# Kernel tuning notes

Measured on AMD Instinct MI355X. Metric: run time of the kernel, lower is better.

## Reference

```python
import jax, jax.numpy as jnp
import numpy as np

B, T, D, W = 8, 2048, 512, 5  # batch, time, hidden_dim, window_size


def setup_inputs() -> dict:
    key = jax.random.key(0)
    k1, k2, k3, k4, k5 = jax.random.split(key, 5)
    outputs = jax.random.normal(k1, (B, T, D), dtype=jnp.float32)
    # torch.nn.Linear default init: U(-1/sqrt(fan_in), 1/sqrt(fan_in))
    s1 = 1.0 / np.sqrt(W * D)
    s2 = 1.0 / np.sqrt((W + 1) * D)
    W_mlp = jax.random.uniform(k2, (D, W * D), jnp.float32, -s1, s1)
    b_mlp = jax.random.uniform(k3, (D,), jnp.float32, -s1, s1)
    W_gate = jax.random.uniform(k4, (D, (W + 1) * D), jnp.float32, -s2, s2)
    b_gate = jax.random.uniform(k5, (D,), jnp.float32, -s2, s2)
    return {"outputs": outputs, "W_mlp": W_mlp, "b_mlp": b_mlp,
            "W_gate": W_gate, "b_gate": b_gate}


def _window_gather(outputs, win):
    """Replicates get_subseq_idx_list + zero padding appended at the end.
    Valid indices are the sorted in-range members of [t-h, t+h]; because
    invalid indices only occur contiguously at the left (t near 0) or right
    (t near T-1) edge, padding-at-end == shift valid entries to the front.
    Returns [B, T, W, D] with zeros in padded slots."""
    Bv, Tv, Dv = outputs.shape
    h = win // 2
    t = jnp.arange(Tv)[:, None]            # [T,1]
    j = jnp.arange(win)[None, :]           # [1,W]
    shift = jnp.maximum(0, h - t)          # left-edge shift
    idx = t - h + j + shift                # [T,W]
    nvalid = jnp.minimum(t + h, Tv - 1) - jnp.maximum(t - h, 0) + 1
    mask = (j < nvalid)                    # [T,W]
    idx = jnp.where(mask, idx, 0)
    winf = outputs[:, idx, :]              # [B,T,W,D]
    return winf * mask[None, :, :, None].astype(outputs.dtype)


def reference(outputs, W_mlp, b_mlp, W_gate, b_gate):
    Bv, Tv, Dv = outputs.shape
    win = W_mlp.shape[1] // Dv             # window size
    scale = 1.0 / jnp.sqrt(jnp.asarray(Dv, outputs.dtype))
    winf = _window_gather(outputs, win)            # [B,T,W,D]
    winf_t = jnp.transpose(winf, (1, 0, 2, 3))     # [T,B,W,D] for scan

    def step(state, w):                            # state: [B,D], w: [B,W,D]
        scores = jnp.einsum('bd,bwd->bw', state, w) * scale
        prob = jax.nn.softmax(scores, axis=-1)     # zeros included, as in torch
        attn = jnp.einsum('bw,bwd->bd', prob, w)   # new prev_state
        flat = w.reshape(Bv, win * Dv)
        mlp = flat @ W_mlp.T + b_mlp
        gate = jax.nn.sigmoid(jnp.concatenate([flat, attn], axis=-1) @ W_gate.T + b_gate)
        out = mlp + attn * gate
        return out, out

    state0 = jnp.zeros((Bv, Dv), dtype=outputs.dtype)
    _, ys = jax.lax.scan(step, state0, winf_t)     # ys: [T,B,D]
    return jnp.transpose(ys, (1, 0, 2))            # [B,T,D]
```

## Files before the change

### kernel.cpp

```cpp
#include <hip/hip_runtime.h>

#define Bq 8
#define Tq 2048
#define Dq 512

typedef __attribute__((ext_vector_type(8))) _Float16 f16x8;
typedef __attribute__((ext_vector_type(8))) short u16x8;
typedef __attribute__((ext_vector_type(4))) float f32x4;

__global__ __launch_bounds__(256) void cvt_f16split(
    const float* __restrict__ s, ushort* __restrict__ hi,
    ushort* __restrict__ lo, int n8) {
  int i = blockIdx.x * 256 + threadIdx.x;
  if (i >= n8) return;
  const float4* sp = reinterpret_cast<const float4*>(s) + i * 2;
  float4 a = sp[0], b = sp[1];
  float x[8] = {a.x, a.y, a.z, a.w, b.x, b.y, b.z, b.w};
  ushort h[8], l[8];
#pragma unroll
  for (int e = 0; e < 8; e++) {
    float xs = x[e] * 256.0f;
    _Float16 hh = (_Float16)xs;
    _Float16 ll = (_Float16)(xs - (float)hh);
    h[e] = *(ushort*)&hh;
    l[e] = *(ushort*)&ll;
  }
  *reinterpret_cast<u16x8*>(hi + (size_t)i * 8) = *reinterpret_cast<u16x8*>(h);
  *reinterpret_cast<u16x8*>(lo + (size_t)i * 8) = *reinterpret_cast<u16x8*>(l);
}

template <int CTRL>
__device__ __forceinline__ float dppadd(float v) {
  int r = __builtin_amdgcn_update_dpp(0, __float_as_int(v), CTRL, 0xF, 0xF, true);
  return v + __int_as_float(r);
}
__device__ __forceinline__ float wave_sum_bcast(float v) {
  v = dppadd<0x111>(v);
  v = dppadd<0x112>(v);
  v = dppadd<0x114>(v);
  v = dppadd<0x118>(v);
  v = dppadd<0x142>(v);
  v = dppadd<0x143>(v);
  return __int_as_float(__builtin_amdgcn_readlane(__float_as_int(v), 63));
}

__device__ __forceinline__ void load_row(const float* __restrict__ base, int r,
                                         int lane, float4& a, float4& b) {
  const float* p = base + (size_t)r * Dq + lane * 4;
  a = *reinterpret_cast<const float4*>(p);
  b = *reinterpret_cast<const float4*>(p + 256);
}

__device__ __forceinline__ float dot8(const float4& xa, const float4& xb,
                                      const float4& ya, const float4& yb) {
  float s = xa.x * ya.x;
  s = fmaf(xa.y, ya.y, s); s = fmaf(xa.z, ya.z, s); s = fmaf(xa.w, ya.w, s);
  s = fmaf(xb.x, yb.x, s); s = fmaf(xb.y, yb.y, s);
  s = fmaf(xb.z, yb.z, s); s = fmaf(xb.w, yb.w, s);
  return s;
}

__device__ __forceinline__ float4 gate_out(const float4& pm, const float4& pg,
                                           const float4& at, const float4& gs) {
  float4 o;
  o.x = fmaf(at.x, __fdividef(1.f, 1.f + __expf(-(pg.x + gs.x))), pm.x);
  o.y = fmaf(at.y, __fdividef(1.f, 1.f + __expf(-(pg.y + gs.y))), pm.y);
  o.z = fmaf(at.z, __fdividef(1.f, 1.f + __expf(-(pg.z + gs.z))), pm.z);
  o.w = fmaf(at.w, __fdividef(1.f, 1.f + __expf(-(pg.w + gs.w))), pm.w);
  return o;
}

#define WSUM4(dst, arr)                                                        \
  dst.x = q0 * arr[S0].x + q1 * arr[S1].x + q2 * arr[S2].x + q3 * arr[S3].x +  \
          q4 * arr[S4].x;                                                      \
  dst.y = q0 * arr[S0].y + q1 * arr[S1].y + q2 * arr[S2].y + q3 * arr[S3].y +  \
          q4 * arr[S4].y;                                                      \
  dst.z = q0 * arr[S0].z + q1 * arr[S1].z + q2 * arr[S2].z + q3 * arr[S3].z +  \
          q4 * arr[S4].z;                                                      \
  dst.w = q0 * arr[S0].w + q1 * arr[S1].w + q2 * arr[S2].w + q3 * arr[S3].w +  \
          q4 * arr[S4].w;

__device__ __forceinline__ void wait_band(int* done, int idx, int target) {
  int it = 0;
  while (__hip_atomic_load(&done[idx], __ATOMIC_ACQUIRE,
                           __HIP_MEMORY_SCOPE_AGENT) < target) {
    __builtin_amdgcn_s_sleep(8);
    if (++it > (1 << 22)) break;
  }
}

template <int S0, int S1, int S2, int S3, int S4, int SLOT, int SLW, bool FLUSH>
__device__ __forceinline__ void scan_step(
    int t, float m3, float m4,
    const float* __restrict__ ob, const float* __restrict__ Gb,
    const float* __restrict__ Pgb, const float* __restrict__ pmb,
    float* __restrict__ po,
    float4 (&owA)[8], float4 (&owB)[8], float4 (&gwA)[8], float4 (&gwB)[8],
    float4 (&pmA)[8], float4 (&pmB)[8], float4 (&pgA)[8], float4 (&pgB)[8],
    float4& stA, float4& stB, int lane, float (*outl)[Dq],
    int* done, int bb, int& bandReady) {
  int rw = t + 5; if (rw > Tq - 1) rw = Tq - 1;
  int band = rw >> 7;
  if (band > bandReady) {
    wait_band(done, bb + band, 12);
    bandReady = band;
  }
  __builtin_amdgcn_sched_barrier(0);
  load_row(ob,  rw, lane, owA[SLW], owB[SLW]);
  load_row(Gb,  rw, lane, gwA[SLW], gwB[SLW]);
  load_row(pmb, rw, lane, pmA[SLW], pmB[SLW]);
  load_row(Pgb, rw, lane, pgA[SLW], pgB[SLW]);
  __builtin_amdgcn_sched_barrier(0);

  float s0 = dot8(stA, stB, owA[S0], owB[S0]);
  float s1 = dot8(stA, stB, owA[S1], owB[S1]);
  float s2 = dot8(stA, stB, owA[S2], owB[S2]);
  float s3 = dot8(stA, stB, owA[S3], owB[S3]);
  float s4 = dot8(stA, stB, owA[S4], owB[S4]);
  const float scale = 0.04419417382415922f;
  s0 = wave_sum_bcast(s0) * scale;
  s1 = wave_sum_bcast(s1) * scale;
  s2 = wave_sum_bcast(s2) * scale;
  s3 = wave_sum_bcast(s3) * (scale * m3);
  s4 = wave_sum_bcast(s4) * (scale * m4);

  float mx = fmaxf(fmaxf(fmaxf(s0, s1), fmaxf(s2, s3)), s4);
  float e0 = __expf(s0 - mx), e1 = __expf(s1 - mx), e2 = __expf(s2 - mx);
  float e3 = __expf(s3 - mx), e4 = __expf(s4 - mx);
  float inv = __fdividef(1.0f, e0 + e1 + e2 + e3 + e4);
  float q0 = e0 * inv, q1 = e1 * inv, q2 = e2 * inv;
  float q3 = e3 * inv * m3, q4 = e4 * inv * m4;

  float4 atA, atB, gsA, gsB;
  WSUM4(atA, owA); WSUM4(atB, owB);
  WSUM4(gsA, gwA); WSUM4(gsB, gwB);

  stA = gate_out(pmA[SLOT], pgA[SLOT], atA, gsA);
  stB = gate_out(pmB[SLOT], pgB[SLOT], atB, gsB);

  reinterpret_cast<float4*>(&outl[SLOT][0])[lane] = stA;
  reinterpret_cast<float4*>(&outl[SLOT][256])[lane] = stB;

  if (FLUSH) {
#pragma unroll
    for (int s = 0; s < 8; s++) {
      float4 va = reinterpret_cast<float4*>(&outl[s][0])[lane];
      float4 vb = reinterpret_cast<float4*>(&outl[s][256])[lane];
      float* dst = po + (size_t)(t - 7 + s) * Dq + lane * 4;
      *reinterpret_cast<float4*>(dst) = va;
      *reinterpret_cast<float4*>(dst + 256) = vb;
    }
  }
}

__global__ __launch_bounds__(256, 1) void fused_kernel(
    const float* __restrict__ O,
    const ushort* __restrict__ Ohi, const ushort* __restrict__ Olo,
    const ushort* __restrict__ Wmh, const ushort* __restrict__ Wml,
    const ushort* __restrict__ Wgh, const ushort* __restrict__ Wgl,
    const float* __restrict__ bm, const float* __restrict__ bg,
    float* __restrict__ Pg, float* __restrict__ Gm,
    float* __restrict__ out, int* __restrict__ done) {
  __shared__ float outl[8][Dq];

  if (blockIdx.x < 8) {
    if (threadIdx.x >= 64) return;
    int b = blockIdx.x;
    int lane = threadIdx.x;
    int bb = b * 16;
    const float* ob  = O   + (size_t)b * Tq * Dq;
    const float* Gb  = Gm  + (size_t)b * Tq * Dq;
    const float* Pgb = Pg  + (size_t)b * Tq * Dq;
    const float* pmb = out + (size_t)b * Tq * Dq;
    float* po = out + (size_t)b * Tq * Dq;

    int bandReady = -1;
    wait_band(done, bb + 0, 12);
    bandReady = 0;
    __builtin_amdgcn_sched_barrier(0);

    float4 owA[8], owB[8], gwA[8], gwB[8], pmA[8], pmB[8], pgA[8], pgB[8];
    float4 stA = make_float4(0.f, 0.f, 0.f, 0.f);
    float4 stB = make_float4(0.f, 0.f, 0.f, 0.f);
#pragma unroll
    for (int r = 0; r < 5; r++) {
      load_row(ob,  r, lane, owA[r], owB[r]);
      load_row(Gb,  r, lane, gwA[r], gwB[r]);
      load_row(pmb, r, lane, pmA[r], pmB[r]);
      load_row(Pgb, r, lane, pgA[r], pgB[r]);
    }

    scan_step<0,1,2,3,4, 0, 5, false>(0, 0.f, 0.f, ob, Gb, Pgb, pmb, po,
        owA,owB,gwA,gwB,pmA,pmB,pgA,pgB, stA,stB, lane, outl, done, bb, bandReady);
    scan_step<0,1,2,3,4, 1, 6, false>(1, 1.f, 0.f, ob, Gb, Pgb, pmb, po,
        owA,owB,gwA,gwB,pmA,pmB,pgA,pgB, stA,stB, lane, outl, done, bb, bandReady);
    for (int tb = 2; tb <= 2034; tb += 8) {
      scan_step<0,1,2,3,4, 2, 7, false>(tb+0, 1.f, 1.f, ob, Gb, Pgb, pmb, po,
          owA,owB,gwA,gwB,pmA,pmB,pgA,pgB, stA,stB, lane, outl, done, bb, bandReady);
      scan_step<1,2,3,4,5, 3, 0, false>(tb+1, 1.f, 1.f, ob, Gb, Pgb, pmb, po,
          owA,owB,gwA,gwB,pmA,pmB,pgA,pgB, stA,stB, lane, outl, done, bb, bandReady);
      scan_step<2,3,4,5,6, 4, 1, false>(tb+2, 1.f, 1.f, ob, Gb, Pgb, pmb, po,
          owA,owB,gwA,gwB,pmA,pmB,pgA,pgB, stA,stB, lane, outl, done, bb, bandReady);
      scan_step<3,4,5,6,7, 5, 2, false>(tb+3, 1.f, 1.f, ob, Gb, Pgb, pmb, po,
          owA,owB,gwA,gwB,pmA,pmB,pgA,pgB, stA,stB, lane, outl, done, bb, bandReady);
      scan_step<4,5,6,7,0, 6, 3, false>(tb+4, 1.f, 1.f, ob, Gb, Pgb, pmb, po,
          owA,owB,gwA,gwB,pmA,pmB,pgA,pgB, stA,stB, lane, outl, done, bb, bandReady);
      scan_step<5,6,7,0,1, 7, 4, true >(tb+5, 1.f, 1.f, ob, Gb, Pgb, pmb, po,
          owA,owB,gwA,gwB,pmA,pmB,pgA,pgB, stA,stB, lane, outl, done, bb, bandReady);
      scan_step<6,7,0,1,2, 0, 5, false>(tb+6, 1.f, 1.f, ob, Gb, Pgb, pmb, po,
          owA,owB,gwA,gwB,pmA,pmB,pgA,pgB, stA,stB, lane, outl, done, bb, bandReady);
      scan_step<7,0,1,2,3, 1, 6, false>(tb+7, 1.f, 1.f, ob, Gb, Pgb, pmb, po,
          owA,owB,gwA,gwB,pmA,pmB,pgA,pgB, stA,stB, lane, outl, done, bb, bandReady);
    }
    scan_step<0,1,2,3,4, 2, 7, false>(2042, 1.f, 1.f, ob, Gb, Pgb, pmb, po,
        owA,owB,gwA,gwB,pmA,pmB,pgA,pgB, stA,stB, lane, outl, done, bb, bandReady);
    scan_step<1,2,3,4,5, 3, 0, false>(2043, 1.f, 1.f, ob, Gb, Pgb, pmb, po,
        owA,owB,gwA,gwB,pmA,pmB,pgA,pgB, stA,stB, lane, outl, done, bb, bandReady);
    scan_step<2,3,4,5,6, 4, 1, false>(2044, 1.f, 1.f, ob, Gb, Pgb, pmb, po,
        owA,owB,gwA,gwB,pmA,pmB,pgA,pgB, stA,stB, lane, outl, done, bb, bandReady);
    scan_step<3,4,5,6,7, 5, 2, false>(2045, 1.f, 1.f, ob, Gb, Pgb, pmb, po,
        owA,owB,gwA,gwB,pmA,pmB,pgA,pgB, stA,stB, lane, outl, done, bb, bandReady);
    scan_step<4,5,6,7,0, 6, 3, false>(2046, 1.f, 0.f, ob, Gb, Pgb, pmb, po,
        owA,owB,gwA,gwB,pmA,pmB,pgA,pgB, stA,stB, lane, outl, done, bb, bandReady);
    scan_step<5,6,7,0,1, 7, 4, true >(2047, 0.f, 0.f, ob, Gb, Pgb, pmb, po,
        owA,owB,gwA,gwB,pmA,pmB,pgA,pgB, stA,stB, lane, outl, done, bb, bandReady);
    return;
  }

  int g = blockIdx.x - 8;
  int band = g / 96;
  int rem = g % 96;
  int bat = rem / 12;
  int role = rem % 12;
  int bt0 = (bat * 16 + band) * 128;
  int gb = bat * Tq;
  int t0 = bt0 % Tq;

  int tid = threadIdx.x;
  int l = tid & 63, w = tid >> 6;
  int wm = w >> 1, wn = w & 1;
  int r16 = l & 15, kg = l >> 4;

  f32x4 acc[4][4] = {};
  const f16x8 zz = {0, 0, 0, 0, 0, 0, 0, 0};

  if (role >= 8) {
    int by = role - 8;
    const ushort *bph[4], *bpl[4];
    int ncol[4];
#pragma unroll
    for (int ni = 0; ni < 4; ni++) {
      int n_g = by * 128 + wn * 64 + ni * 16 + r16;
      ncol[ni] = n_g;
      size_t off = (size_t)n_g * 3072 + 2560 + kg * 8;
      bph[ni] = Wgh + off; bpl[ni] = Wgl + off;
    }
    const ushort *aph[4], *apl[4];
#pragma unroll
    for (int mi = 0; mi < 4; mi++) {
      size_t off = (size_t)(bt0 + wm * 64 + mi * 16 + r16) * Dq + kg * 8;
      aph[mi] = Ohi + off; apl[mi] = Olo + off;
    }
#pragma unroll 4
    for (int ks = 0; ks < 16; ks++) {
      f16x8 Ah[4], Al[4], Bh[4], Bl[4];
#pragma unroll
      for (int mi = 0; mi < 4; mi++) {
        Ah[mi] = *(const f16x8*)aph[mi]; aph[mi] += 32;
        Al[mi] = *(const f16x8*)apl[mi]; apl[mi] += 32;
      }
#pragma unroll
      for (int ni = 0; ni < 4; ni++) {
        Bh[ni] = *(const f16x8*)bph[ni]; bph[ni] += 32;
        Bl[ni] = *(const f16x8*)bpl[ni]; bpl[ni] += 32;
      }
#pragma unroll
      for (int mi = 0; mi < 4; mi++)
#pragma unroll
        for (int ni = 0; ni < 4; ni++) {
          acc[mi][ni] = __builtin_amdgcn_mfma_f32_16x16x32_f16(Ah[mi], Bh[ni], acc[mi][ni], 0, 0, 0);
          acc[mi][ni] = __builtin_amdgcn_mfma_f32_16x16x32_f16(Al[mi], Bh[ni], acc[mi][ni], 0, 0, 0);
          acc[mi][ni] = __builtin_amdgcn_mfma_f32_16x16x32_f16(Ah[mi], Bl[ni], acc[mi][ni], 0, 0, 0);
        }
    }
    const float SC = 1.0f / 65536.0f;
#pragma unroll
    for (int ni = 0; ni < 4; ni++) {
#pragma unroll
      for (int mi = 0; mi < 4; mi++) {
        int rowb = bt0 + wm * 64 + mi * 16 + kg * 4;
#pragma unroll
        for (int rr = 0; rr < 4; rr++)
          Gm[(size_t)(rowb + rr) * Dq + ncol[ni]] = acc[mi][ni][rr] * SC;
      }
    }
  } else {
    int by = role;
    const ushort *bph[4], *bpl[4];
    int ncol[4];
#pragma unroll
    for (int ni = 0; ni < 4; ni++) {
      int n_g = by * 128 + wn * 64 + ni * 16 + r16;
      ncol[ni] = n_g;
      size_t off;
      if (by < 4) { off = (size_t)n_g * 2560 + kg * 8; bph[ni] = Wmh + off; bpl[ni] = Wml + off; }
      else { off = (size_t)(n_g - 512) * 3072 + kg * 8; bph[ni] = Wgh + off; bpl[ni] = Wgl + off; }
    }
    int arow[4][5];
    uint vmask[4];
#pragma unroll
    for (int mi = 0; mi < 4; mi++) {
      int t = t0 + wm * 64 + mi * 16 + r16;
      int sh = 2 - t; if (sh < 0) sh = 0;
      int hi2 = t + 2; if (hi2 > Tq - 1) hi2 = Tq - 1;
      int lo2 = t - 2; if (lo2 < 0) lo2 = 0;
      int nv = hi2 - lo2 + 1;
      uint vm = 0;
#pragma unroll
      for (int j = 0; j < 5; j++) {
        int r = t - 2 + j + sh;
        if (r > Tq - 1) r = Tq - 1;
        arow[mi][j] = gb + r;
        if (j < nv) vm |= (1u << j);
      }
      vmask[mi] = vm;
    }
#pragma unroll
    for (int j = 0; j < 5; j++) {
      const ushort *aph[4], *apl[4];
      bool v[4];
#pragma unroll
      for (int mi = 0; mi < 4; mi++) {
        size_t off = (size_t)arow[mi][j] * Dq + kg * 8;
        aph[mi] = Ohi + off; apl[mi] = Olo + off;
        v[mi] = (vmask[mi] >> j) & 1u;
      }
#pragma unroll 4
      for (int ks = 0; ks < 16; ks++) {
        f16x8 Ah[4], Al[4], Bh[4], Bl[4];
#pragma unroll
        for (int mi = 0; mi < 4; mi++) {
          f16x8 th = *(const f16x8*)aph[mi]; aph[mi] += 32;
          f16x8 tl = *(const f16x8*)apl[mi]; apl[mi] += 32;
          Ah[mi] = v[mi] ? th : zz;
          Al[mi] = v[mi] ? tl : zz;
        }
#pragma unroll
        for (int ni = 0; ni < 4; ni++) {
          Bh[ni] = *(const f16x8*)bph[ni]; bph[ni] += 32;
          Bl[ni] = *(const f16x8*)bpl[ni]; bpl[ni] += 32;
        }
#pragma unroll
        for (int mi = 0; mi < 4; mi++)
#pragma unroll
          for (int ni = 0; ni < 4; ni++) {
            acc[mi][ni] = __builtin_amdgcn_mfma_f32_16x16x32_f16(Ah[mi], Bh[ni], acc[mi][ni], 0, 0, 0);
            acc[mi][ni] = __builtin_amdgcn_mfma_f32_16x16x32_f16(Al[mi], Bh[ni], acc[mi][ni], 0, 0, 0);
            acc[mi][ni] = __builtin_amdgcn_mfma_f32_16x16x32_f16(Ah[mi], Bl[ni], acc[mi][ni], 0, 0, 0);
          }
      }
    }
    const float SC = 1.0f / 65536.0f;
    float* dst = (by < 4) ? out : Pg;
    const float* bias = (by < 4) ? bm : bg;
#pragma unroll
    for (int ni = 0; ni < 4; ni++) {
      int oc = (by < 4) ? ncol[ni] : ncol[ni] - 512;
      float bi = bias[oc];
#pragma unroll
      for (int mi = 0; mi < 4; mi++) {
        int rowb = bt0 + wm * 64 + mi * 16 + kg * 4;
#pragma unroll
        for (int rr = 0; rr < 4; rr++)
          dst[(size_t)(rowb + rr) * Dq + oc] = fmaf(acc[mi][ni][rr], SC, bi);
      }
    }
  }

  __threadfence();
  __syncthreads();
  if (tid == 0) {
    __hip_atomic_fetch_add(&done[bat * 16 + band], 1, __ATOMIC_RELEASE,
                           __HIP_MEMORY_SCOPE_AGENT);
  }
}

__global__ __launch_bounds__(256) void gemm_pre(
    const float* __restrict__ O, const float* __restrict__ Wm,
    const float* __restrict__ Wg, const float* __restrict__ bm,
    const float* __restrict__ bg, float* __restrict__ Pm,
    float* __restrict__ Pg, float* __restrict__ Gm, int mode) {
  const int BM = 128, BN = 128, BK = 16;
  __shared__ float As[BK][132];
  __shared__ float Bs[BK][132];
  int tidx = threadIdx.x;
  int bt0 = blockIdx.x * BM;
  int b = bt0 / Tq;
  int t0 = bt0 % Tq;
  int n0 = blockIdx.y * BN;
  int K = mode ? Dq : 5 * Dq;
  int tx = tidx % 16, ty = tidx / 16, lr = tidx >> 2, lc = (tidx & 3) * 4;
  float acc[8][8];
#pragma unroll
  for (int i = 0; i < 8; i++)
#pragma unroll
    for (int j = 0; j < 8; j++) acc[i][j] = 0.f;
  for (int kb = 0; kb < K; kb += BK) {
#pragma unroll
    for (int h = 0; h < 2; h++) {
      int m = lr + h * 64;
      int t = t0 + m;
      float4 av;
      if (mode == 0) {
        int j = kb >> 9;
        int kcol = (kb & 511) + lc;
        int sh = 2 - t; if (sh < 0) sh = 0;
        int r = t - 2 + j + sh;
        int hi = t + 2; if (hi > Tq - 1) hi = Tq - 1;
        int lo2 = t - 2; if (lo2 < 0) lo2 = 0;
        int nv = hi - lo2 + 1;
        if (j < nv) av = *reinterpret_cast<const float4*>(O + ((size_t)b * Tq + r) * Dq + kcol);
        else av = make_float4(0.f, 0.f, 0.f, 0.f);
      } else {
        av = *reinterpret_cast<const float4*>(O + ((size_t)b * Tq + t) * Dq + kb + lc);
      }
      As[lc + 0][m] = av.x; As[lc + 1][m] = av.y;
      As[lc + 2][m] = av.z; As[lc + 3][m] = av.w;
    }
#pragma unroll
    for (int h = 0; h < 2; h++) {
      int n = lr + h * 64;
      int gn = n0 + n;
      const float* wrow;
      int col;
      if (mode == 0) {
        if (gn < 512) { wrow = Wm + (size_t)gn * 2560; col = kb + lc; }
        else          { wrow = Wg + (size_t)(gn - 512) * 3072; col = kb + lc; }
      } else {
        wrow = Wg + (size_t)gn * 3072; col = 2560 + kb + lc;
      }
      float4 bv = *reinterpret_cast<const float4*>(wrow + col);
      Bs[lc + 0][n] = bv.x; Bs[lc + 1][n] = bv.y;
      Bs[lc + 2][n] = bv.z; Bs[lc + 3][n] = bv.w;
    }
    __syncthreads();
#pragma unroll
    for (int kk = 0; kk < BK; kk++) {
      float a[8], bb[8];
      float4 a0 = *reinterpret_cast<float4*>(&As[kk][ty * 8]);
      float4 a1 = *reinterpret_cast<float4*>(&As[kk][ty * 8 + 4]);
      float4 b0 = *reinterpret_cast<float4*>(&Bs[kk][tx * 8]);
      float4 b1 = *reinterpret_cast<float4*>(&Bs[kk][tx * 8 + 4]);
      a[0]=a0.x; a[1]=a0.y; a[2]=a0.z; a[3]=a0.w; a[4]=a1.x; a[5]=a1.y; a[6]=a1.z; a[7]=a1.w;
      bb[0]=b0.x; bb[1]=b0.y; bb[2]=b0.z; bb[3]=b0.w; bb[4]=b1.x; bb[5]=b1.y; bb[6]=b1.z; bb[7]=b1.w;
#pragma unroll
      for (int i = 0; i < 8; i++)
#pragma unroll
        for (int j = 0; j < 8; j++) acc[i][j] = fmaf(a[i], bb[j], acc[i][j]);
    }
    __syncthreads();
  }
  int gn = n0 + tx * 8;
  float bias[8];
  float* dstbase;
  int coloff;
  if (mode == 0) {
    if (gn < 512) {
#pragma unroll
      for (int j = 0; j < 8; j++) bias[j] = bm[gn + j];
      dstbase = Pm; coloff = gn;
    } else {
#pragma unroll
      for (int j = 0; j < 8; j++) bias[j] = bg[gn - 512 + j];
      dstbase = Pg; coloff = gn - 512;
    }
  } else {
#pragma unroll
    for (int j = 0; j < 8; j++) bias[j] = 0.f;
    dstbase = Gm; coloff = gn;
  }
#pragma unroll
  for (int i = 0; i < 8; i++) {
    int bt = bt0 + ty * 8 + i;
    float4 v0 = make_float4(acc[i][0] + bias[0], acc[i][1] + bias[1],
                            acc[i][2] + bias[2], acc[i][3] + bias[3]);
    float4 v1 = make_float4(acc[i][4] + bias[4], acc[i][5] + bias[5],
                            acc[i][6] + bias[6], acc[i][7] + bias[7]);
    float4* d = reinterpret_cast<float4*>(dstbase + (size_t)bt * Dq + coloff);
    d[0] = v0;
    d[1] = v1;
  }
}

__global__ __launch_bounds__(64, 1) void scan_only(
    const float* __restrict__ O, const float* __restrict__ Gm,
    const float* __restrict__ Pg, const float* __restrict__ Pm,
    float* __restrict__ out, int* __restrict__ done) {
  __shared__ float outl[8][Dq];
  int b = blockIdx.x;
  int lane = threadIdx.x;
  int bb = b * 16;
  const float* ob  = O  + (size_t)b * Tq * Dq;
  const float* Gb  = Gm + (size_t)b * Tq * Dq;
  const float* Pgb = Pg + (size_t)b * Tq * Dq;
  const float* pmb = Pm + (size_t)b * Tq * Dq;
  float* po = out + (size_t)b * Tq * Dq;
  int bandReady = 15;

  float4 owA[8], owB[8], gwA[8], gwB[8], pmA[8], pmB[8], pgA[8], pgB[8];
  float4 stA = make_float4(0.f, 0.f, 0.f, 0.f);
  float4 stB = make_float4(0.f, 0.f, 0.f, 0.f);
#pragma unroll
  for (int r = 0; r < 5; r++) {
    load_row(ob,  r, lane, owA[r], owB[r]);
    load_row(Gb,  r, lane, gwA[r], gwB[r]);
    load_row(pmb, r, lane, pmA[r], pmB[r]);
    load_row(Pgb, r, lane, pgA[r], pgB[r]);
  }
  scan_step<0,1,2,3,4, 0, 5, false>(0, 0.f, 0.f, ob, Gb, Pgb, pmb, po,
      owA,owB,gwA,gwB,pmA,pmB,pgA,pgB, stA,stB, lane, outl, done, bb, bandReady);
  scan_step<0,1,2,3,4, 1, 6, false>(1, 1.f, 0.f, ob, Gb, Pgb, pmb, po,
      owA,owB,gwA,gwB,pmA,pmB,pgA,pgB, stA,stB, lane, outl, done, bb, bandReady);
  for (int tb = 2; tb <= 2034; tb += 8) {
    scan_step<0,1,2,3,4, 2, 7, false>(tb+0, 1.f, 1.f, ob, Gb, Pgb, pmb, po,
        owA,owB,gwA,gwB,pmA,pmB,pgA,pgB, stA,stB, lane, outl, done, bb, bandReady);
    scan_step<1,2,3,4,5, 3, 0, false>(tb+1, 1.f, 1.f, ob, Gb, Pgb, pmb, po,
        owA,owB,gwA,gwB,pmA,pmB,pgA,pgB, stA,stB, lane, outl, done, bb, bandReady);
    scan_step<2,3,4,5,6, 4, 1, false>(tb+2, 1.f, 1.f, ob, Gb, Pgb, pmb, po,
        owA,owB,gwA,gwB,pmA,pmB,pgA,pgB, stA,stB, lane, outl, done, bb, bandReady);
    scan_step<3,4,5,6,7, 5, 2, false>(tb+3, 1.f, 1.f, ob, Gb, Pgb, pmb, po,
        owA,owB,gwA,gwB,pmA,pmB,pgA,pgB, stA,stB, lane, outl, done, bb, bandReady);
    scan_step<4,5,6,7,0, 6, 3, false>(tb+4, 1.f, 1.f, ob, Gb, Pgb, pmb, po,
        owA,owB,gwA,gwB,pmA,pmB,pgA,pgB, stA,stB, lane, outl, done, bb, bandReady);
    scan_step<5,6,7,0,1, 7, 4, true >(tb+5, 1.f, 1.f, ob, Gb, Pgb, pmb, po,
        owA,owB,gwA,gwB,pmA,pmB,pgA,pgB, stA,stB, lane, outl, done, bb, bandReady);
    scan_step<6,7,0,1,2, 0, 5, false>(tb+6, 1.f, 1.f, ob, Gb, Pgb, pmb, po,
        owA,owB,gwA,gwB,pmA,pmB,pgA,pgB, stA,stB, lane, outl, done, bb, bandReady);
    scan_step<7,0,1,2,3, 1, 6, false>(tb+7, 1.f, 1.f, ob, Gb, Pgb, pmb, po,
        owA,owB,gwA,gwB,pmA,pmB,pgA,pgB, stA,stB, lane, outl, done, bb, bandReady);
  }
  scan_step<0,1,2,3,4, 2, 7, false>(2042, 1.f, 1.f, ob, Gb, Pgb, pmb, po,
      owA,owB,gwA,gwB,pmA,pmB,pgA,pgB, stA,stB, lane, outl, done, bb, bandReady);
  scan_step<1,2,3,4,5, 3, 0, false>(2043, 1.f, 1.f, ob, Gb, Pgb, pmb, po,
      owA,owB,gwA,gwB,pmA,pmB,pgA,pgB, stA,stB, lane, outl, done, bb, bandReady);
  scan_step<2,3,4,5,6, 4, 1, false>(2044, 1.f, 1.f, ob, Gb, Pgb, pmb, po,
      owA,owB,gwA,gwB,pmA,pmB,pgA,pgB, stA,stB, lane, outl, done, bb, bandReady);
  scan_step<3,4,5,6,7, 5, 2, false>(2045, 1.f, 1.f, ob, Gb, Pgb, pmb, po,
      owA,owB,gwA,gwB,pmA,pmB,pgA,pgB, stA,stB, lane, outl, done, bb, bandReady);
  scan_step<4,5,6,7,0, 6, 3, false>(2046, 1.f, 0.f, ob, Gb, Pgb, pmb, po,
      owA,owB,gwA,gwB,pmA,pmB,pgA,pgB, stA,stB, lane, outl, done, bb, bandReady);
  scan_step<5,6,7,0,1, 7, 4, true >(2047, 0.f, 0.f, ob, Gb, Pgb, pmb, po,
      owA,owB,gwA,gwB,pmA,pmB,pgA,pgB, stA,stB, lane, outl, done, bb, bandReady);
}

extern "C" void kernel_launch(void* const* d_in, const int* in_sizes, int n_in,
                              void* d_out, int out_size, void* d_ws, size_t ws_size,
                              hipStream_t stream) {
  const float* O  = (const float*)d_in[0];
  const float* Wm = (const float*)d_in[1];
  const float* bm = (const float*)d_in[2];
  const float* Wg = (const float*)d_in[3];
  const float* bg = (const float*)d_in[4];
  float* out = (float*)d_out;

  const size_t NTOT = (size_t)Bq * Tq * Dq;
  const size_t NWM = 512 * 2560, NWG = 512 * 3072;
  float* Pg = (float*)d_ws;
  float* Gm = Pg + NTOT;
  ushort* OHI = (ushort*)(Gm + NTOT);
  ushort* OLO = OHI + NTOT;
  ushort* WMH = OLO + NTOT;
  ushort* WML = WMH + NWM;
  ushort* WGH = WML + NWM;
  ushort* WGL = WGH + NWG;
  int* done = (int*)(WGL + NWG);

  size_t need = 2 * NTOT * 4 + 2 * (NTOT + NWM + NWG) * 2 + 128 * 4;
  if (ws_size >= need) {
    hipMemsetAsync(done, 0, 128 * 4, stream);
    cvt_f16split<<<dim3((NTOT / 8 + 255) / 256), dim3(256), 0, stream>>>(O, OHI, OLO, NTOT / 8);
    cvt_f16split<<<dim3((NWM / 8 + 255) / 256), dim3(256), 0, stream>>>(Wm, WMH, WML, NWM / 8);
    cvt_f16split<<<dim3((NWG / 8 + 255) / 256), dim3(256), 0, stream>>>(Wg, WGH, WGL, NWG / 8);
    fused_kernel<<<dim3(8 + 16 * 96), dim3(256), 0, stream>>>(
        O, OHI, OLO, WMH, WML, WGH, WGL, bm, bg, Pg, Gm, out, done);
  } else {
    bool sep = ws_size >= (size_t)(3 * NTOT * 4 + 128 * 4);
    float* Pm = sep ? (Gm + NTOT) : out;
    int* done2 = sep ? (int*)(Pm + NTOT) : (int*)(Gm + NTOT);
    hipMemsetAsync(done2, 12, 128 * 4, stream);
    gemm_pre<<<dim3(128, 8), dim3(256), 0, stream>>>(O, Wm, Wg, bm, bg, Pm, Pg, Gm, 0);
    gemm_pre<<<dim3(128, 4), dim3(256), 0, stream>>>(O, Wm, Wg, bm, bg, Pm, Pg, Gm, 1);
    scan_only<<<dim3(Bq), dim3(64), 0, stream>>>(O, Gm, Pg, Pm, out, done2);
  }
}
```

Baseline: 1.779 ms.

## Split recurrent scan across four waves with LDS cross-wave score reduction

The sequential scan per batch now uses all four waves of the block instead of one. Each wave handles 128 of the 512 hidden dims and each thread holds two elements rather than eight. The five attention scores are reduced within each wave, exchanged through a small double-buffered shared array, and combined after a block barrier on every timestep. The LDS output staging and periodic flush are dropped in favour of a direct float2 store per step. This cuts per-thread work and register pressure on the latency-bound recurrence, at the cost of a block-wide barrier and an LDS round trip on every step.

```diff
diff --git a/kernel.cpp b/kernel.cpp
--- a/kernel.cpp
+++ b/kernel.cpp
@@ -44,42 +44,6 @@
   return __int_as_float(__builtin_amdgcn_readlane(__float_as_int(v), 63));
 }
 
-__device__ __forceinline__ void load_row(const float* __restrict__ base, int r,
-                                         int lane, float4& a, float4& b) {
-  const float* p = base + (size_t)r * Dq + lane * 4;
-  a = *reinterpret_cast<const float4*>(p);
-  b = *reinterpret_cast<const float4*>(p + 256);
-}
-
-__device__ __forceinline__ float dot8(const float4& xa, const float4& xb,
-                                      const float4& ya, const float4& yb) {
-  float s = xa.x * ya.x;
-  s = fmaf(xa.y, ya.y, s); s = fmaf(xa.z, ya.z, s); s = fmaf(xa.w, ya.w, s);
-  s = fmaf(xb.x, yb.x, s); s = fmaf(xb.y, yb.y, s);
-  s = fmaf(xb.z, yb.z, s); s = fmaf(xb.w, yb.w, s);
-  return s;
-}
-
-__device__ __forceinline__ float4 gate_out(const float4& pm, const float4& pg,
-                                           const float4& at, const float4& gs) {
-  float4 o;
-  o.x = fmaf(at.x, __fdividef(1.f, 1.f + __expf(-(pg.x + gs.x))), pm.x);
-  o.y = fmaf(at.y, __fdividef(1.f, 1.f + __expf(-(pg.y + gs.y))), pm.y);
-  o.z = fmaf(at.z, __fdividef(1.f, 1.f + __expf(-(pg.z + gs.z))), pm.z);
-  o.w = fmaf(at.w, __fdividef(1.f, 1.f + __expf(-(pg.w + gs.w))), pm.w);
-  return o;
-}
-
-#define WSUM4(dst, arr)                                                        \
-  dst.x = q0 * arr[S0].x + q1 * arr[S1].x + q2 * arr[S2].x + q3 * arr[S3].x +  \
-          q4 * arr[S4].x;                                                      \
-  dst.y = q0 * arr[S0].y + q1 * arr[S1].y + q2 * arr[S2].y + q3 * arr[S3].y +  \
-          q4 * arr[S4].y;                                                      \
-  dst.z = q0 * arr[S0].z + q1 * arr[S1].z + q2 * arr[S2].z + q3 * arr[S3].z +  \
-          q4 * arr[S4].z;                                                      \
-  dst.w = q0 * arr[S0].w + q1 * arr[S1].w + q2 * arr[S2].w + q3 * arr[S3].w +  \
-          q4 * arr[S4].w;
-
 __device__ __forceinline__ void wait_band(int* done, int idx, int target) {
   int it = 0;
   while (__hip_atomic_load(&done[idx], __ATOMIC_ACQUIRE,
@@ -89,16 +53,15 @@
   }
 }
 
-template <int S0, int S1, int S2, int S3, int S4, int SLOT, int SLW, bool FLUSH>
-__device__ __forceinline__ void scan_step(
-    int t, float m3, float m4,
+template <int S0, int S1, int S2, int S3, int S4, int SLOT, int SLW>
+__device__ __forceinline__ void scan_step4(
+    int t, float m3, float m4, int lane, int w, int dbase,
     const float* __restrict__ ob, const float* __restrict__ Gb,
     const float* __restrict__ Pgb, const float* __restrict__ pmb,
-    float* __restrict__ po,
-    float4 (&owA)[8], float4 (&owB)[8], float4 (&gwA)[8], float4 (&gwB)[8],
-    float4 (&pmA)[8], float4 (&pmB)[8], float4 (&pgA)[8], float4 (&pgB)[8],
-    float4& stA, float4& stB, int lane, float (*outl)[Dq],
-    int* done, int bb, int& bandReady) {
+    float* __restrict__ po, float (*red)[5][4],
+    int* done, int bb, int& bandReady,
+    float2 (&ow)[8], float2 (&gw)[8], float2 (&pm)[8], float2 (&pg)[8],
+    float2& st) {
   int rw = t + 5; if (rw > Tq - 1) rw = Tq - 1;
   int band = rw >> 7;
   if (band > bandReady) {
@@ -106,51 +69,66 @@
     bandReady = band;
   }
   __builtin_amdgcn_sched_barrier(0);
-  load_row(ob,  rw, lane, owA[SLW], owB[SLW]);
-  load_row(Gb,  rw, lane, gwA[SLW], gwB[SLW]);
-  load_row(pmb, rw, lane, pmA[SLW], pmB[SLW]);
-  load_row(Pgb, rw, lane, pgA[SLW], pgB[SLW]);
+  ow[SLW] = *(const float2*)(ob  + (size_t)rw * Dq + dbase);
+  gw[SLW] = *(const float2*)(Gb  + (size_t)rw * Dq + dbase);
+  pm[SLW] = *(const float2*)(pmb + (size_t)rw * Dq + dbase);
+  pg[SLW] = *(const float2*)(Pgb + (size_t)rw * Dq + dbase);
   __builtin_amdgcn_sched_barrier(0);
 
-  float s0 = dot8(stA, stB, owA[S0], owB[S0]);
-  float s1 = dot8(stA, stB, owA[S1], owB[S1]);
-  float s2 = dot8(stA, stB, owA[S2], owB[S2]);
-  float s3 = dot8(stA, stB, owA[S3], owB[S3]);
-  float s4 = dot8(stA, stB, owA[S4], owB[S4]);
   const float scale = 0.04419417382415922f;
-  s0 = wave_sum_bcast(s0) * scale;
-  s1 = wave_sum_bcast(s1) * scale;
-  s2 = wave_sum_bcast(s2) * scale;
-  s3 = wave_sum_bcast(s3) * (scale * m3);
-  s4 = wave_sum_bcast(s4) * (scale * m4);
-
-  float mx = fmaxf(fmaxf(fmaxf(s0, s1), fmaxf(s2, s3)), s4);
-  float e0 = __expf(s0 - mx), e1 = __expf(s1 - mx), e2 = __expf(s2 - mx);
-  float e3 = __expf(s3 - mx), e4 = __expf(s4 - mx);
+  float s0 = st.x * ow[S0].x; s0 = fmaf(st.y, ow[S0].y, s0);
+  float s1 = st.x * ow[S1].x; s1 = fmaf(st.y, ow[S1].y, s1);
+  float s2 = st.x * ow[S2].x; s2 = fmaf(st.y, ow[S2].y, s2);
+  float s3 = st.x * ow[S3].x; s3 = fmaf(st.y, ow[S3].y, s3);
+  float s4 = st.x * ow[S4].x; s4 = fmaf(st.y, ow[S4].y, s4);
+  s0 = wave_sum_bcast(s0);
+  s1 = wave_sum_bcast(s1);
+  s2 = wave_sum_bcast(s2);
+  s3 = wave_sum_bcast(s3);
+  s4 = wave_sum_bcast(s4);
+  s0 *= scale; s1 *= scale; s2 *= scale;
+  s3 *= scale * m3;
+  s4 *= scale * m4;
+
+  float pv = s0;
+  pv = (lane == 1) ? s1 : pv;
+  pv = (lane == 2) ? s2 : pv;
+  pv = (lane == 3) ? s3 : pv;
+  pv = (lane == 4) ? s4 : pv;
+  if (lane < 5) red[t & 1][lane][w] = pv;
+
+  asm volatile("s_waitcnt lgkmcnt(0)" ::: "memory");
+  __builtin_amdgcn_sched_barrier(0);
+  __builtin_amdgcn_s_barrier();
+  __builtin_amdgcn_sched_barrier(0);
+
+  float fs[5];
+#pragma unroll
+  for (int j = 0; j < 5; j++) {
+    float4 rv = *(const float4*)(&red[t & 1][j][0]);
+    fs[j] = (rv.x + rv.y) + (rv.z + rv.w);
+  }
+  float mx = fmaxf(fmaxf(fmaxf(fs[0], fs[1]), fmaxf(fs[2], fs[3])), fs[4]);
+  float e0 = __expf(fs[0] - mx), e1 = __expf(fs[1] - mx), e2 = __expf(fs[2] - mx);
+  float e3 = __expf(fs[3] - mx), e4 = __expf(fs[4] - mx);
   float inv = __fdividef(1.0f, e0 + e1 + e2 + e3 + e4);
   float q0 = e0 * inv, q1 = e1 * inv, q2 = e2 * inv;
   float q3 = e3 * inv * m3, q4 = e4 * inv * m4;
 
-  float4 atA, atB, gsA, gsB;
-  WSUM4(atA, owA); WSUM4(atB, owB);
-  WSUM4(gsA, gwA); WSUM4(gsB, gwB);
-
-  stA = gate_out(pmA[SLOT], pgA[SLOT], atA, gsA);
-  stB = gate_out(pmB[SLOT], pgB[SLOT], atB, gsB);
-
-  reinterpret_cast<float4*>(&outl[SLOT][0])[lane] = stA;
-  reinterpret_cast<float4*>(&outl[SLOT][256])[lane] = stB;
-
-  if (FLUSH) {
-#pragma unroll
-    for (int s = 0; s < 8; s++) {
-      float4 va = reinterpret_cast<float4*>(&outl[s][0])[lane];
-      float4 vb = reinterpret_cast<float4*>(&outl[s][256])[lane];
-      float* dst = po + (size_t)(t - 7 + s) * Dq + lane * 4;
-      *reinterpret_cast<float4*>(dst) = va;
-      *reinterpret_cast<float4*>(dst + 256) = vb;
-    }
-  }
+  float ax = q0 * ow[S0].x; ax = fmaf(q1, ow[S1].x, ax); ax = fmaf(q2, ow[S2].x, ax);
+  ax = fmaf(q3, ow[S3].x, ax); ax = fmaf(q4, ow[S4].x, ax);
+  float ay = q0 * ow[S0].y; ay = fmaf(q1, ow[S1].y, ay); ay = fmaf(q2, ow[S2].y, ay);
+  ay = fmaf(q3, ow[S3].y, ay); ay = fmaf(q4, ow[S4].y, ay);
+  float gx = q0 * gw[S0].x; gx = fmaf(q1, gw[S1].x, gx); gx = fmaf(q2, gw[S2].x, gx);
+  gx = fmaf(q3, gw[S3].x, gx); gx = fmaf(q4, gw[S4].x, gx);
+  float gy = q0 * gw[S0].y; gy = fmaf(q1, gw[S1].y, gy); gy = fmaf(q2, gw[S2].y, gy);
+  gy = fmaf(q3, gw[S3].y, gy); gy = fmaf(q4, gw[S4].y, gy);
+
+  float2 ot;
+  ot.x = fmaf(ax, __fdividef(1.f, 1.f + __expf(-(pg[SLOT].x + gx))), pm[SLOT].x);
+  ot.y = fmaf(ay, __fdividef(1.f, 1.f + __expf(-(pg[SLOT].y + gy))), pm[SLOT].y);
+  st = ot;
+  *(float2*)(po + (size_t)t * Dq + dbase) = ot;
 }
 
 __global__ __launch_bounds__(256, 1) void fused_kernel(
@@ -161,12 +139,14 @@
     const float* __restrict__ bm, const float* __restrict__ bg,
     float* __restrict__ Pg, float* __restrict__ Gm,
     float* __restrict__ out, int* __restrict__ done) {
-  __shared__ float outl[8][Dq];
+  __shared__ __align__(16) float red[2][5][4];
 
   if (blockIdx.x < 8) {
-    if (threadIdx.x >= 64) return;
     int b = blockIdx.x;
-    int lane = threadIdx.x;
+    int tid = threadIdx.x;
+    int w = tid >> 6;
+    int lane = tid & 63;
+    int dbase = w * 128 + lane * 2;
     int bb = b * 16;
     const float* ob  = O   + (size_t)b * Tq * Dq;
     const float* Gb  = Gm  + (size_t)b * Tq * Dq;
@@ -179,51 +159,39 @@
     bandReady = 0;
     __builtin_amdgcn_sched_barrier(0);
 
-    float4 owA[8], owB[8], gwA[8], gwB[8], pmA[8], pmB[8], pgA[8], pgB[8];
-    float4 stA = make_float4(0.f, 0.f, 0.f, 0.f);
-    float4 stB = make_float4(0.f, 0.f, 0.f, 0.f);
+    float2 ow[8], gw[8], pm[8], pg[8];
+    float2 st = make_float2(0.f, 0.f);
 #pragma unroll
     for (int r = 0; r < 5; r++) {
-      load_row(ob,  r, lane, owA[r], owB[r]);
-      load_row(Gb,  r, lane, gwA[r], gwB[r]);
-      load_row(pmb, r, lane, pmA[r], pmB[r]);
-      load_row(Pgb, r, lane, pgA[r], pgB[r]);
-    }
-
-    scan_step<0,1,2,3,4, 0, 5, false>(0, 0.f, 0.f, ob, Gb, Pgb, pmb, po,
-        owA,owB,gwA,gwB,pmA,pmB,pgA,pgB, stA,stB, lane, outl, done, bb, bandReady);
-    scan_step<0,1,2,3,4, 1, 6, false>(1, 1.f, 0.f, ob, Gb, Pgb, pmb, po,
-        owA,owB,gwA,gwB,pmA,pmB,pgA,pgB, stA,stB, lane, outl, done, bb, bandReady);
+      ow[r] = *(const float2*)(ob  + (size_t)r * Dq + dbase);
+      gw[r] = *(const float2*)(Gb  + (size_t)r * Dq + dbase);
+      pm[r] = *(const float2*)(pmb + (size_t)r * Dq + dbase);
+      pg[r] = *(const float2*)(Pgb + (size_t)r * Dq + dbase);
+    }
+
+#define SS(t_, m3_, m4_, A,B,C,D,E, SL_, LW_)                                  \
+    scan_step4<A,B,C,D,E, SL_, LW_>(t_, m3_, m4_, lane, w, dbase, ob, Gb,      \
+        Pgb, pmb, po, red, done, bb, bandReady, ow, gw, pm, pg, st)
+
+    SS(0, 0.f, 0.f, 0,1,2,3,4, 0, 5);
+    SS(1, 1.f, 0.f, 0,1,2,3,4, 1, 6);
     for (int tb = 2; tb <= 2034; tb += 8) {
-      scan_step<0,1,2,3,4, 2, 7, false>(tb+0, 1.f, 1.f, ob, Gb, Pgb, pmb, po,
-          owA,owB,gwA,gwB,pmA,pmB,pgA,pgB, stA,stB, lane, outl, done, bb, bandReady);
-      scan_step<1,2,3,4,5, 3, 0, false>(tb+1, 1.f, 1.f, ob, Gb, Pgb, pmb, po,
-          owA,owB,gwA,gwB,pmA,pmB,pgA,pgB, stA,stB, lane, outl, done, bb, bandReady);
-      scan_step<2,3,4,5,6, 4, 1, false>(tb+2, 1.f, 1.f, ob, Gb, Pgb, pmb, po,
-          owA,owB,gwA,gwB,pmA,pmB,pgA,pgB, stA,stB, lane, outl, done, bb, bandReady);
-      scan_step<3,4,5,6,7, 5, 2, false>(tb+3, 1.f, 1.f, ob, Gb, Pgb, pmb, po,
-          owA,owB,gwA,gwB,pmA,pmB,pgA,pgB, stA,stB, lane, outl, done, bb, bandReady);
-      scan_step<4,5,6,7,0, 6, 3, false>(tb+4, 1.f, 1.f, ob, Gb, Pgb, pmb, po,
-          owA,owB,gwA,gwB,pmA,pmB,pgA,pgB, stA,stB, lane, outl, done, bb, bandReady);
-      scan_step<5,6,7,0,1, 7, 4, true >(tb+5, 1.f, 1.f, ob, Gb, Pgb, pmb, po,
-          owA,owB,gwA,gwB,pmA,pmB,pgA,pgB, stA,stB, lane, outl, done, bb, bandReady);
-      scan_step<6,7,0,1,2, 0, 5, false>(tb+6, 1.f, 1.f, ob, Gb, Pgb, pmb, po,
-          owA,owB,gwA,gwB,pmA,pmB,pgA,pgB, stA,stB, lane, outl, done, bb, bandReady);
-      scan_step<7,0,1,2,3, 1, 6, false>(tb+7, 1.f, 1.f, ob, Gb, Pgb, pmb, po,
-          owA,owB,gwA,gwB,pmA,pmB,pgA,pgB, stA,stB, lane, outl, done, bb, bandReady);
-    }
-    scan_step<0,1,2,3,4, 2, 7, false>(2042, 1.f, 1.f, ob, Gb, Pgb, pmb, po,
-        owA,owB,gwA,gwB,pmA,pmB,pgA,pgB, stA,stB, lane, outl, done, bb, bandReady);
-    scan_step<1,2,3,4,5, 3, 0, false>(2043, 1.f, 1.f, ob, Gb, Pgb, pmb, po,
-        owA,owB,gwA,gwB,pmA,pmB,pgA,pgB, stA,stB, lane, outl, done, bb, bandReady);
-    scan_step<2,3,4,5,6, 4, 1, false>(2044, 1.f, 1.f, ob, Gb, Pgb, pmb, po,
-        owA,owB,gwA,gwB,pmA,pmB,pgA,pgB, stA,stB, lane, outl, done, bb, bandReady);
-    scan_step<3,4,5,6,7, 5, 2, false>(2045, 1.f, 1.f, ob, Gb, Pgb, pmb, po,
-        owA,owB,gwA,gwB,pmA,pmB,pgA,pgB, stA,stB, lane, outl, done, bb, bandReady);
-    scan_step<4,5,6,7,0, 6, 3, false>(2046, 1.f, 0.f, ob, Gb, Pgb, pmb, po,
-        owA,owB,gwA,gwB,pmA,pmB,pgA,pgB, stA,stB, lane, outl, done, bb, bandReady);
-    scan_step<5,6,7,0,1, 7, 4, true >(2047, 0.f, 0.f, ob, Gb, Pgb, pmb, po,
-        owA,owB,gwA,gwB,pmA,pmB,pgA,pgB, stA,stB, lane, outl, done, bb, bandReady);
+      SS(tb+0, 1.f, 1.f, 0,1,2,3,4, 2, 7);
+      SS(tb+1, 1.f, 1.f, 1,2,3,4,5, 3, 0);
+      SS(tb+2, 1.f, 1.f, 2,3,4,5,6, 4, 1);
+      SS(tb+3, 1.f, 1.f, 3,4,5,6,7, 5, 2);
+      SS(tb+4, 1.f, 1.f, 4,5,6,7,0, 6, 3);
+      SS(tb+5, 1.f, 1.f, 5,6,7,0,1, 7, 4);
+      SS(tb+6, 1.f, 1.f, 6,7,0,1,2, 0, 5);
+      SS(tb+7, 1.f, 1.f, 7,0,1,2,3, 1, 6);
+    }
+    SS(2042, 1.f, 1.f, 0,1,2,3,4, 2, 7);
+    SS(2043, 1.f, 1.f, 1,2,3,4,5, 3, 0);
+    SS(2044, 1.f, 1.f, 2,3,4,5,6, 4, 1);
+    SS(2045, 1.f, 1.f, 3,4,5,6,7, 5, 2);
+    SS(2046, 1.f, 0.f, 4,5,6,7,0, 6, 3);
+    SS(2047, 0.f, 0.f, 5,6,7,0,1, 7, 4);
+#undef SS
     return;
   }
 
@@ -492,13 +460,16 @@
   }
 }
 
-__global__ __launch_bounds__(64, 1) void scan_only(
+__global__ __launch_bounds__(256, 1) void scan_only(
     const float* __restrict__ O, const float* __restrict__ Gm,
     const float* __restrict__ Pg, const float* __restrict__ Pm,
     float* __restrict__ out, int* __restrict__ done) {
-  __shared__ float outl[8][Dq];
+  __shared__ __align__(16) float red[2][5][4];
   int b = blockIdx.x;
-  int lane = threadIdx.x;
+  int tid = threadIdx.x;
+  int w = tid >> 6;
+  int lane = tid & 63;
+  int dbase = w * 128 + lane * 2;
   int bb = b * 16;
   const float* ob  = O  + (size_t)b * Tq * Dq;
   const float* Gb  = Gm + (size_t)b * Tq * Dq;
@@ -507,50 +478,37 @@
   float* po = out + (size_t)b * Tq * Dq;
   int bandReady = 15;
 
-  float4 owA[8], owB[8], gwA[8], gwB[8], pmA[8], pmB[8], pgA[8], pgB[8];
-  float4 stA = make_float4(0.f, 0.f, 0.f, 0.f);
-  float4 stB = make_float4(0.f, 0.f, 0.f, 0.f);
+  float2 ow[8], gw[8], pm[8], pg[8];
+  float2 st = make_float2(0.f, 0.f);
 #pragma unroll
   for (int r = 0; r < 5; r++) {
-    load_row(ob,  r, lane, owA[r], owB[r]);
-    load_row(Gb,  r, lane, gwA[r], gwB[r]);
-    load_row(pmb, r, lane, pmA[r], pmB[r]);
-    load_row(Pgb, r, lane, pgA[r], pgB[r]);
-  }
-  scan_step<0,1,2,3,4, 0, 5, false>(0, 0.f, 0.f, ob, Gb, Pgb, pmb, po,
-      owA,owB,gwA,gwB,pmA,pmB,pgA,pgB, stA,stB, lane, outl, done, bb, bandReady);
-  scan_step<0,1,2,3,4, 1, 6, false>(1, 1.f, 0.f, ob, Gb, Pgb, pmb, po,
-      owA,owB,gwA,gwB,pmA,pmB,pgA,pgB, stA,stB, lane, outl, done, bb, bandReady);
+    ow[r] = *(const float2*)(ob  + (size_t)r * Dq + dbase);
+    gw[r] = *(const float2*)(Gb  + (size_t)r * Dq + dbase);
+    pm[r] = *(const float2*)(pmb + (size_t)r * Dq + dbase);
+    pg[r] = *(const float2*)(Pgb + (size_t)r * Dq + dbase);
+  }
+#define SS(t_, m3_, m4_, A,B,C,D,E, SL_, LW_)                                  \
+  scan_step4<A,B,C,D,E, SL_, LW_>(t_, m3_, m4_, lane, w, dbase, ob, Gb,        \
+      Pgb, pmb, po, red, done, bb, bandReady, ow, gw, pm, pg, st)
+  SS(0, 0.f, 0.f, 0,1,2,3,4, 0, 5);
+  SS(1, 1.f, 0.f, 0,1,2,3,4, 1, 6);
   for (int tb = 2; tb <= 2034; tb += 8) {
-    scan_step<0,1,2,3,4, 2, 7, false>(tb+0, 1.f, 1.f, ob, Gb, Pgb, pmb, po,
-        owA,owB,gwA,gwB,pmA,pmB,pgA,pgB, stA,stB, lane, outl, done, bb, bandReady);
-    scan_step<1,2,3,4,5, 3, 0, false>(tb+1, 1.f, 1.f, ob, Gb, Pgb, pmb, po,
-        owA,owB,gwA,gwB,pmA,pmB,pgA,pgB, stA,stB, lane, outl, done, bb, bandReady);
-    scan_step<2,3,4,5,6, 4, 1, false>(tb+2, 1.f, 1.f, ob, Gb, Pgb, pmb, po,
-        owA,owB,gwA,gwB,pmA,pmB,pgA,pgB, stA,stB, lane, outl, done, bb, bandReady);
-    scan_step<3,4,5,6,7, 5, 2, false>(tb+3, 1.f, 1.f, ob, Gb, Pgb, pmb, po,
-        owA,owB,gwA,gwB,pmA,pmB,pgA,pgB, stA,stB, lane, outl, done, bb, bandReady);
-    scan_step<4,5,6,7,0, 6, 3, false>(tb+4, 1.f, 1.f, ob, Gb, Pgb, pmb, po,
-        owA,owB,gwA,gwB,pmA,pmB,pgA,pgB, stA,stB, lane, outl, done, bb, bandReady);
-    scan_step<5,6,7,0,1, 7, 4, true >(tb+5, 1.f, 1.f, ob, Gb, Pgb, pmb, po,
-        owA,owB,gwA,gwB,pmA,pmB,pgA,pgB, stA,stB, lane, outl, done, bb, bandReady);
-    scan_step<6,7,0,1,2, 0, 5, false>(tb+6, 1.f, 1.f, ob, Gb, Pgb, pmb, po,
-        owA,owB,gwA,gwB,pmA,pmB,pgA,pgB, stA,stB, lane, outl, done, bb, bandReady);
-    scan_step<7,0,1,2,3, 1, 6, false>(tb+7, 1.f, 1.f, ob, Gb, Pgb, pmb, po,
-        owA,owB,gwA,gwB,pmA,pmB,pgA,pgB, stA,stB, lane, outl, done, bb, bandReady);
-  }
-  scan_step<0,1,2,3,4, 2, 7, false>(2042, 1.f, 1.f, ob, Gb, Pgb, pmb, po,
-      owA,owB,gwA,gwB,pmA,pmB,pgA,pgB, stA,stB, lane, outl, done, bb, bandReady);
-  scan_step<1,2,3,4,5, 3, 0, false>(2043, 1.f, 1.f, ob, Gb, Pgb, pmb, po,
-      owA,owB,gwA,gwB,pmA,pmB,pgA,pgB, stA,stB, lane, outl, done, bb, bandReady);
-  scan_step<2,3,4,5,6, 4, 1, false>(2044, 1.f, 1.f, ob, Gb, Pgb, pmb, po,
-      owA,owB,gwA,gwB,pmA,pmB,pgA,pgB, stA,stB, lane, outl, done, bb, bandReady);
-  scan_step<3,4,5,6,7, 5, 2, false>(2045, 1.f, 1.f, ob, Gb, Pgb, pmb, po,
-      owA,owB,gwA,gwB,pmA,pmB,pgA,pgB, stA,stB, lane, outl, done, bb, bandReady);
-  scan_step<4,5,6,7,0, 6, 3, false>(2046, 1.f, 0.f, ob, Gb, Pgb, pmb, po,
-      owA,owB,gwA,gwB,pmA,pmB,pgA,pgB, stA,stB, lane, outl, done, bb, bandReady);
-  scan_step<5,6,7,0,1, 7, 4, true >(2047, 0.f, 0.f, ob, Gb, Pgb, pmb, po,
-      owA,owB,gwA,gwB,pmA,pmB,pgA,pgB, stA,stB, lane, outl, done, bb, bandReady);
+    SS(tb+0, 1.f, 1.f, 0,1,2,3,4, 2, 7);
+    SS(tb+1, 1.f, 1.f, 1,2,3,4,5, 3, 0);
+    SS(tb+2, 1.f, 1.f, 2,3,4,5,6, 4, 1);
+    SS(tb+3, 1.f, 1.f, 3,4,5,6,7, 5, 2);
+    SS(tb+4, 1.f, 1.f, 4,5,6,7,0, 6, 3);
+    SS(tb+5, 1.f, 1.f, 5,6,7,0,1, 7, 4);
+    SS(tb+6, 1.f, 1.f, 6,7,0,1,2, 0, 5);
+    SS(tb+7, 1.f, 1.f, 7,0,1,2,3, 1, 6);
+  }
+  SS(2042, 1.f, 1.f, 0,1,2,3,4, 2, 7);
+  SS(2043, 1.f, 1.f, 1,2,3,4,5, 3, 0);
+  SS(2044, 1.f, 1.f, 2,3,4,5,6, 4, 1);
+  SS(2045, 1.f, 1.f, 3,4,5,6,7, 5, 2);
+  SS(2046, 1.f, 0.f, 4,5,6,7,0, 6, 3);
+  SS(2047, 0.f, 0.f, 5,6,7,0,1, 7, 4);
+#undef SS
 }
 
 extern "C" void kernel_launch(void* const* d_in, const int* in_sizes, int n_in,
@@ -590,6 +548,6 @@
     hipMemsetAsync(done2, 12, 128 * 4, stream);
     gemm_pre<<<dim3(128, 8), dim3(256), 0, stream>>>(O, Wm, Wg, bm, bg, Pm, Pg, Gm, 0);
     gemm_pre<<<dim3(128, 4), dim3(256), 0, stream>>>(O, Wm, Wg, bm, bg, Pm, Pg, Gm, 1);
-    scan_only<<<dim3(Bq), dim3(64), 0, stream>>>(O, Gm, Pg, Pm, out, done2);
-  }
-}
+    scan_only<<<dim3(Bq), dim3(256), 0, stream>>>(O, Gm, Pg, Pm, out, done2);
+  }
+}
```

Result: no change. 1.779 ms (-0.0%).
